# Optimization experiments

Measured on AMD Instinct MI355X. Metric: run time of the kernel, lower is better.

## Reference

```python
import jax, jax.numpy as jnp
import numpy as np

B = 8
RESOLUTIONS = [65, 129, 257, 513, 1025]
NUM_POINTS = [0, 4096, 16384, 65536, 262144]
CLIP_MIN = -1e9
FINAL = 1025          # last resolution (both axes)
B_MIN, B_MAX = -1.0, 1.0
BALANCE = 0.5


def setup_inputs() -> dict:
    key = jax.random.key(0)
    k1, k2, k3, k4 = jax.random.split(key, 4)
    return {
        "w1": jax.random.normal(k1, (2, 256), jnp.float32),
        "b1": jax.random.normal(k2, (256,), jnp.float32),
        "w2": jax.random.normal(k3, (256, 1), jnp.float32),
        "b2": jax.random.normal(k4, (1,), jnp.float32),
    }


def _interp_bilinear_ac(x, H, W):
    """F.interpolate(..., mode='bilinear', align_corners=True). x: [B, C, h, w]."""
    b, c, h, w = x.shape
    ys = jnp.linspace(0.0, h - 1.0, H)
    xs = jnp.linspace(0.0, w - 1.0, W)
    y0 = jnp.floor(ys).astype(jnp.int32)
    y1 = jnp.minimum(y0 + 1, h - 1)
    wy = ys - y0
    x0 = jnp.floor(xs).astype(jnp.int32)
    x1 = jnp.minimum(x0 + 1, w - 1)
    wx = xs - x0
    # interpolate rows, then columns
    top = x[:, :, y0, :] * (1.0 - wy)[None, None, :, None] + x[:, :, y1, :] * wy[None, None, :, None]
    return top[:, :, :, x0] * (1.0 - wx) + top[:, :, :, x1] * wx


def _batch_eval(coords, w1, b1, w2, b2):
    """coords: [B, N, 2] in final-resolution pixel space (align_corners=False mapping).
    Returns occupancy [B, N] (C == 1)."""
    coords2d = coords / FINAL + 0.5 / FINAL                 # normalize to [0, 1]
    p = coords2d * (B_MAX - B_MIN) + B_MIN                  # [B, N, 2] in world coords
    h = jax.nn.relu(jnp.einsum('bnd,dh->bnh', p, w1) + b1)  # [B, N, 256]
    occ = jax.nn.sigmoid(jnp.einsum('bnh,ho->bno', h, w2) + b2)
    return occ[..., 0]


def reference(w1, b1, w2, b2):
    occ = None
    for i, res in enumerate(RESOLUTIONS):
        if i == 0:
            # init_coords: grid of res x res points spanning [0, FINAL-1]
            xs = jnp.linspace(0.0, FINAL - 1.0, res)
            gy, gx = jnp.meshgrid(xs, xs, indexing='ij')          # y rows, x cols
            coords = jnp.stack([gx.ravel(), gy.ravel()], axis=-1)  # [N, 2] (x, y)
            coords = jnp.broadcast_to(coords, (B, res * res, 2))
            o = _batch_eval(coords, w1, b1, w2, b2)               # [B, N]
            occ = o.reshape(B, 1, res, res)                       # [B, C, H, W]
        else:
            occ = _interp_bilinear_ac(occ, res, res)
            npt = NUM_POINTS[i]
            if npt <= 0:
                continue
            # uncertainty = -|occ - balance_value|
            unc = -jnp.abs(occ - BALANCE)                          # [B, 1, H, W]
            flat_unc = unc.reshape(B, res * res)
            scores, idx = jax.lax.top_k(flat_unc, npt)             # [B, npt]
            px = (idx % res).astype(jnp.float32)
            py = (idx // res).astype(jnp.float32)
            stride = (FINAL - 1.0) / (res - 1.0)
            coords = jnp.stack([px, py], axis=-1) * stride         # [B, npt, 2]
            new_vals = _batch_eval(coords, w1, b1, w2, b2)         # [B, npt]
            occ_flat = occ.reshape(B, res * res)
            old_vals = jnp.take_along_axis(occ_flat, idx, axis=1)
            vals = jnp.where(scores >= CLIP_MIN, new_vals, old_vals)
            occ_flat = jax.vmap(lambda o, i2, v: o.at[i2].set(v))(occ_flat, idx, vals)
            occ = occ_flat.reshape(B, 1, res, res)
    return occ
```

## Files before the change

### kernel.cpp

```cpp
#include <hip/hip_runtime.h>
#include <stdint.h>

#define HID 256
#define NMAXPIX (1025 * 1025)
#define NREP 8
#define NSEG 2048
#define SELMAX 2112

#define HISTA_OFF 0
#define HISTB_OFF 16384
#define HISTC_OFF 32768
#define SCAL_OFF  40960
#define TIC_OFF   41024
#define STAGE_U32 43072

__device__ __forceinline__ float mlp_eval4(float wx, float wy,
                                           const float4* __restrict__ w1x,
                                           const float4* __restrict__ w1y,
                                           const float4* __restrict__ vb1,
                                           const float4* __restrict__ vw2, float b2v) {
    const float C0 = (float)(0.5 / 1025.0);
    float px = (wx / 1025.0f + C0) * 2.0f - 1.0f;
    float py = (wy / 1025.0f + C0) * 2.0f - 1.0f;
    float a0 = 0.f, a1 = 0.f, a2 = 0.f, a3 = 0.f;
#pragma unroll 8
    for (int q = 0; q < HID / 4; ++q) {
        float4 a = w1x[q], b = w1y[q], c = vb1[q], d = vw2[q];
        float h0 = px * a.x + py * b.x + c.x;
        float h1 = px * a.y + py * b.y + c.y;
        float h2 = px * a.z + py * b.z + c.z;
        float h3 = px * a.w + py * b.w + c.w;
        h0 = h0 > 0.f ? h0 : 0.f;
        h1 = h1 > 0.f ? h1 : 0.f;
        h2 = h2 > 0.f ? h2 : 0.f;
        h3 = h3 > 0.f ? h3 : 0.f;
        a0 += h0 * d.x;
        a1 += h1 * d.y;
        a2 += h2 * d.z;
        a3 += h3 * d.w;
    }
    float x = ((a0 + a1) + (a2 + a3)) + b2v;
    float r;
    if (x >= 0.f) { r = 1.0f / (1.0f + expf(-x)); }
    else { float e = expf(x); r = e / (1.0f + e); }
    return r;
}

__device__ __forceinline__ uint32_t block_exscan_256(uint32_t v, volatile uint32_t* lds4) {
    int lane = threadIdx.x & 63, w = threadIdx.x >> 6;
    uint32_t inc = v;
#pragma unroll
    for (int d = 1; d < 64; d <<= 1) {
        uint32_t o = (uint32_t)__shfl_up((int)inc, d, 64);
        if (lane >= d) inc += o;
    }
    if (lane == 63) lds4[w] = inc;
    __syncthreads();
    uint32_t woff = 0;
    for (int i = 0; i < w; ++i) woff += lds4[i];
    return woff + inc - v;
}

__device__ void scan_generic(const uint32_t* __restrict__ hist, int NB, int nrep,
                             uint32_t rem_in, uint32_t prefix_in, int shift,
                             uint32_t* outp, uint32_t* outr,
                             volatile uint32_t* lds4, volatile uint32_t* ldspair) {
    int tid = threadIdx.x;
    int C = NB >> 8;
    int b0 = NB - (tid + 1) * C;
    uint32_t cnts[8];
#pragma unroll
    for (int k = 0; k < 8; ++k) cnts[k] = 0;
    for (int rep = 0; rep < nrep; ++rep) {
        const uint4* p = (const uint4*)(hist + (size_t)rep * NB + b0);
#pragma unroll
        for (int g = 0; g < 2; ++g) {
            if (g * 4 < C) {
                uint4 v = p[g];
                cnts[g * 4 + 0] += v.x;
                cnts[g * 4 + 1] += v.y;
                cnts[g * 4 + 2] += v.z;
                cnts[g * 4 + 3] += v.w;
            }
        }
    }
    uint32_t ssum = 0;
    for (int k = 0; k < C; ++k) ssum += cnts[k];
    uint32_t excl = block_exscan_256(ssum, lds4);
    uint32_t run = excl;
    for (int k = 0; k < C; ++k) {
        uint32_t c = cnts[C - 1 - k];
        if (rem_in > run && rem_in <= run + c) {
            ldspair[0] = (prefix_in << shift) | (uint32_t)(b0 + C - 1 - k);
            ldspair[1] = rem_in - run;
        }
        run += c;
    }
    __syncthreads();
    *outp = ldspair[0];
    *outr = ldspair[1];
}

__device__ __forceinline__ void hist_add(uint32_t* lh, uint32_t bin, bool act, int lane) {
    unsigned long long m = __ballot(act);
    if (m) {
        int leader = __ffsll(m) - 1;
        uint32_t lbin = (uint32_t)__shfl((int)bin, leader, 64);
        unsigned long long smk = __ballot(act && bin == lbin);
        if (smk == m) {
            if (lane == leader) atomicAdd(&lh[lbin], (uint32_t)__popcll(m));
        } else if (act) {
            atomicAdd(&lh[bin], 1u);
        }
    }
}

__device__ __forceinline__ float up2x(const float* __restrict__ in, int rp, int r, int n) {
    int i = n / r, j = n % r;
    int i2 = i >> 1, j2 = j >> 1;
    float v;
    if ((i & 1) == 0) {
        if ((j & 1) == 0) {
            v = in[i2 * rp + j2];
        } else {
            float a = in[i2 * rp + j2], b = in[i2 * rp + j2 + 1];
            v = a * 0.5f + b * 0.5f;
        }
    } else {
        if ((j & 1) == 0) {
            float a = in[i2 * rp + j2], b = in[(i2 + 1) * rp + j2];
            v = a * 0.5f + b * 0.5f;
        } else {
            float a = in[i2 * rp + j2],      c = in[i2 * rp + j2 + 1];
            float b = in[(i2 + 1) * rp + j2], d = in[(i2 + 1) * rp + j2 + 1];
            float t1 = a * 0.5f + b * 0.5f;
            float t2 = c * 0.5f + d * 0.5f;
            v = t1 * 0.5f + t2 * 0.5f;
        }
    }
    return v;
}

__global__ __launch_bounds__(256) void k_eval0z(const float* __restrict__ w1, const float* __restrict__ b1,
                                                const float* __restrict__ w2, const float* __restrict__ b2,
                                                float* __restrict__ occ, uint32_t* __restrict__ zbuf, int zcount) {
    __shared__ alignas(16) float sw1[2 * HID];
    __shared__ alignas(16) float sb1[HID];
    __shared__ alignas(16) float sw2[HID];
    int tid = threadIdx.x;
    for (int i = tid; i < 2 * HID; i += 256) sw1[i] = w1[i];
    sb1[tid] = b1[tid];
    sw2[tid] = w2[tid];
    __syncthreads();
    int gtid = blockIdx.x * 256 + tid;
    int nthreads = gridDim.x * 256;
    for (int i = gtid; i < zcount; i += nthreads) zbuf[i] = 0;
    for (int n = gtid; n < 65 * 65; n += nthreads) {
        int i = n / 65, j = n % 65;
        occ[n] = mlp_eval4(16.0f * (float)j, 16.0f * (float)i,
                           (const float4*)sw1, (const float4*)(sw1 + HID),
                           (const float4*)sb1, (const float4*)sw2, b2[0]);
    }
}

__global__ __launch_bounds__(256) void k_upkey(const float* __restrict__ in, int rp,
                                               float* __restrict__ outg, int r, int nb, int bstride,
                                               uint32_t* __restrict__ keys,
                                               uint32_t* __restrict__ histA) {
    __shared__ uint32_t hist[2048];
    int tid = threadIdx.x;
    for (int k = tid; k < 2048; k += 256) hist[k] = 0;
    __syncthreads();
    int N = r * r;
    int lane = tid & 63;
    int gstride = gridDim.x * 256;
    for (int n0 = blockIdx.x * 256; n0 < N; n0 += gstride) {
        int n = n0 + tid;
        bool act = n < N;
        uint32_t key = 0;
        if (act) {
            float v = up2x(in, rp, r, n);
            for (int k = 0; k < nb; ++k) outg[(size_t)k * bstride + n] = v;
            float unc = -fabsf(v - 0.5f);
            uint32_t u = __float_as_uint(unc);
            key = (u & 0x80000000u) ? ~u : (u | 0x80000000u);
            keys[n] = key;
        }
        hist_add(hist, key >> 21, act, lane);
    }
    __syncthreads();
    uint32_t* myrep = histA + (size_t)(blockIdx.x & (NREP - 1)) * 2048;
    for (int k = tid; k < 2048; k += 256) {
        uint32_t c = hist[k];
        if (c) atomicAdd(&myrep[k], c);
    }
}

__global__ __launch_bounds__(256) void k_histmid(const uint32_t* __restrict__ keys, int N,
                                                 const uint32_t* __restrict__ prevHist,
                                                 uint32_t* __restrict__ scal,
                                                 int useNpt, uint32_t npt, int scalInIdx, int shift,
                                                 int scalOutIdx,
                                                 int fshift, int bshift, uint32_t bmask,
                                                 uint32_t* __restrict__ outHist, int NBout) {
    __shared__ uint32_t lh[2048];
    __shared__ uint32_t lds4[4];
    __shared__ uint32_t ldspair[2];
    int tid = threadIdx.x, lane = tid & 63;
    uint32_t rem_in = useNpt ? npt : scal[scalInIdx + 1];
    uint32_t pfx_in = useNpt ? 0u  : scal[scalInIdx];
    uint32_t pfx, rem;
    scan_generic(prevHist, 2048, NREP, rem_in, pfx_in, shift, &pfx, &rem, lds4, ldspair);
    if (blockIdx.x == 0 && tid == 0) { scal[scalOutIdx] = pfx; scal[scalOutIdx + 1] = rem; }
    for (int k = tid; k < 2048; k += 256) lh[k] = 0;
    __syncthreads();
    int gstride = gridDim.x * 256;
    for (int base = blockIdx.x * 256; base < N; base += gstride) {
        int n = base + tid;
        bool inb = n < N;
        uint32_t key = inb ? keys[n] : 0u;
        bool flt = inb && ((key >> fshift) == pfx);
        uint32_t bin = (key >> bshift) & bmask;
        hist_add(lh, bin, flt, lane);
    }
    __syncthreads();
    uint32_t* myrep = outHist + (size_t)(blockIdx.x & (NREP - 1)) * NBout;
    for (int k = tid; k < NBout; k += 256) {
        uint32_t c = lh[k];
        if (c) atomicAdd(&myrep[k], c);
    }
}

__global__ __launch_bounds__(256, 2) void k_segsel(
        const uint32_t* __restrict__ keys, int N, int seglen,
        const uint32_t* __restrict__ histC,
        const uint32_t* __restrict__ scal,
        uint32_t* __restrict__ tic,
        int r, float stride,
        float* __restrict__ occ, int nb, int bstride,
        const float* __restrict__ w1, const float* __restrict__ b1,
        const float* __restrict__ w2, const float* __restrict__ b2) {
    __shared__ alignas(16) float sw1[2 * HID];
    __shared__ alignas(16) float sb1[HID];
    __shared__ alignas(16) float sw2[HID];
    __shared__ uint32_t selcnt;
    __shared__ uint32_t selidx[SELMAX];
    __shared__ uint32_t lds4[4];
    __shared__ uint32_t ldspair[2];
    __shared__ uint32_t wtc[4];
    __shared__ uint32_t s_excl;
    int tid = threadIdx.x, lane = tid & 63, w = tid >> 6;
    for (int i = tid; i < 2 * HID; i += 256) sw1[i] = w1[i];
    sb1[tid] = b1[tid];
    sw2[tid] = w2[tid];
    if (tid == 0) { selcnt = 0; s_excl = 0; }

    uint32_t rem2 = scal[3], pfx2 = scal[2];
    uint32_t K, t;
    scan_generic(histC, 1024, NREP, rem2, pfx2, 10, &K, &t, lds4, ldspair);

    int wv = blockIdx.x * 4 + w;
    int s0 = wv * seglen;
    int s1 = s0 + seglen; if (s1 > N) s1 = N;
    uint32_t tcnt = 0;
    for (int base = s0; base < s1; base += 64) {
        int n = base + lane;
        if (n < s1) tcnt += (keys[n] == K) ? 1u : 0u;
    }
#pragma unroll
    for (int d = 32; d; d >>= 1) tcnt += (uint32_t)__shfl_down((int)tcnt, d, 64);
    if (lane == 0) wtc[w] = tcnt;
    __syncthreads();
    uint32_t agg = wtc[0] + wtc[1] + wtc[2] + wtc[3];
    uint32_t intra = 0;
    for (int i = 0; i < w; ++i) intra += wtc[i];

    if (tid == 0) {
        uint32_t st = (blockIdx.x == 0) ? ((2u << 30) | agg) : ((1u << 30) | agg);
        __hip_atomic_store(&tic[blockIdx.x], st, __ATOMIC_RELAXED, __HIP_MEMORY_SCOPE_AGENT);
    }
    if (blockIdx.x > 0 && w == 0) {
        uint32_t excl = 0;
        int b = (int)blockIdx.x - 1;
        for (;;) {
            int mine = b - lane;
            bool active = (mine >= 0);
            uint32_t f = 0;
            if (active) {
                f = __hip_atomic_load(&tic[mine], __ATOMIC_RELAXED, __HIP_MEMORY_SCOPE_AGENT);
                int spins = 0;
                while ((f >> 30) == 0u && spins < 1000) {
                    __builtin_amdgcn_s_sleep(2);
                    f = __hip_atomic_load(&tic[mine], __ATOMIC_RELAXED, __HIP_MEMORY_SCOPE_AGENT);
                    ++spins;
                }
                if ((f >> 30) == 0u) {
                    int ms0 = mine * seglen;
                    int ms1 = ms0 + seglen; if (ms1 > N) ms1 = N;
                    uint32_t c = 0;
                    for (int n2 = ms0; n2 < ms1; ++n2) c += (keys[n2] == K) ? 1u : 0u;
                    f = (1u << 30) | c;
                }
            }
            unsigned long long incm = __ballot(active && (f >> 30) == 2u);
            uint32_t val;
            bool done = (incm != 0ull);
            if (done) {
                int l2 = __ffsll(incm) - 1;
                val = (lane <= l2) ? (f & 0x3FFFFFFFu) : 0u;
            } else {
                val = active ? (f & 0x3FFFFFFFu) : 0u;
            }
#pragma unroll
            for (int d = 32; d; d >>= 1) val += (uint32_t)__shfl_down((int)val, d, 64);
            val = (uint32_t)__shfl((int)val, 0, 64);
            excl += val;
            if (done) break;
            if (b < 64) break;
            b -= 64;
        }
        if (lane == 0) {
            __hip_atomic_store(&tic[blockIdx.x], (2u << 30) | (excl + agg),
                               __ATOMIC_RELAXED, __HIP_MEMORY_SCOPE_AGENT);
            s_excl = excl;
        }
    }
    __syncthreads();
    uint32_t tie_run = s_excl + intra;

    unsigned long long lowmask = (lane == 63) ? ~0ull >> 1 : ((1ull << lane) - 1ull);
    for (int base = s0; base < s1; base += 64) {
        int n = base + lane;
        bool inb = n < s1;
        uint32_t key = inb ? keys[n] : 0u;
        bool gt = inb && (key > K);
        bool tie = inb && (key == K);
        unsigned long long tm = __ballot(tie);
        uint32_t trank = tie_run + (uint32_t)__popcll(tm & lowmask);
        bool sel = gt || (tie && trank < t);
        unsigned long long smk = __ballot(sel);
        if (smk) {
            int leader = __ffsll(smk) - 1;
            uint32_t wbase = 0;
            if (lane == leader) wbase = atomicAdd(&selcnt, (uint32_t)__popcll(smk));
            wbase = (uint32_t)__shfl((int)wbase, leader, 64);
            if (sel) selidx[wbase + (uint32_t)__popcll(smk & lowmask)] = (uint32_t)n;
        }
        tie_run += (uint32_t)__popcll(tm);
    }
    __syncthreads();

    uint32_t cnt = selcnt;
    float vb2 = b2[0];
    const float4* w1x = (const float4*)sw1;
    const float4* w1y = (const float4*)(sw1 + HID);
    const float4* vb1 = (const float4*)sb1;
    const float4* vw2 = (const float4*)sw2;
    const float C0 = (float)(0.5 / 1025.0);
    for (uint32_t bb = 0; bb < cnt; bb += 512) {
        uint32_t i0 = bb + tid, i1 = bb + tid + 256;
        bool v0 = i0 < cnt, v1 = i1 < cnt;
        int nA = v0 ? (int)selidx[i0] : 0;
        int nB = v1 ? (int)selidx[i1] : 0;
        int iA = nA / r, jA = nA % r;
        int iB = nB / r, jB = nB % r;
        float pxA = ((stride * (float)jA) / 1025.0f + C0) * 2.0f - 1.0f;
        float pyA = ((stride * (float)iA) / 1025.0f + C0) * 2.0f - 1.0f;
        float pxB = ((stride * (float)jB) / 1025.0f + C0) * 2.0f - 1.0f;
        float pyB = ((stride * (float)iB) / 1025.0f + C0) * 2.0f - 1.0f;
        float4 A0 = {0, 0, 0, 0}, A1 = {0, 0, 0, 0};
#pragma unroll 4
        for (int q = 0; q < HID / 4; ++q) {
            float4 a = w1x[q], b = w1y[q], c = vb1[q], d = vw2[q];
            {
                float h0 = pxA * a.x + pyA * b.x + c.x;
                float h1 = pxA * a.y + pyA * b.y + c.y;
                float h2 = pxA * a.z + pyA * b.z + c.z;
                float h3 = pxA * a.w + pyA * b.w + c.w;
                h0 = h0 > 0.f ? h0 : 0.f;
                h1 = h1 > 0.f ? h1 : 0.f;
                h2 = h2 > 0.f ? h2 : 0.f;
                h3 = h3 > 0.f ? h3 : 0.f;
                A0.x += h0 * d.x; A0.y += h1 * d.y;
                A0.z += h2 * d.z; A0.w += h3 * d.w;
            }
            {
                float h0 = pxB * a.x + pyB * b.x + c.x;
                float h1 = pxB * a.y + pyB * b.y + c.y;
                float h2 = pxB * a.z + pyB * b.z + c.z;
                float h3 = pxB * a.w + pyB * b.w + c.w;
                h0 = h0 > 0.f ? h0 : 0.f;
                h1 = h1 > 0.f ? h1 : 0.f;
                h2 = h2 > 0.f ? h2 : 0.f;
                h3 = h3 > 0.f ? h3 : 0.f;
                A1.x += h0 * d.x; A1.y += h1 * d.y;
                A1.z += h2 * d.z; A1.w += h3 * d.w;
            }
        }
        if (v0) {
            float x = ((A0.x + A0.y) + (A0.z + A0.w)) + vb2;
            float rr;
            if (x >= 0.f) { rr = 1.0f / (1.0f + expf(-x)); }
            else { float e = expf(x); rr = e / (1.0f + e); }
            for (int k = 0; k < nb; ++k) occ[(size_t)k * bstride + nA] = rr;
        }
        if (v1) {
            float x = ((A1.x + A1.y) + (A1.z + A1.w)) + vb2;
            float rr;
            if (x >= 0.f) { rr = 1.0f / (1.0f + expf(-x)); }
            else { float e = expf(x); rr = e / (1.0f + e); }
            for (int k = 0; k < nb; ++k) occ[(size_t)k * bstride + nB] = rr;
        }
    }
}

__global__ __launch_bounds__(256) void k_bcast(const float* __restrict__ src, float* __restrict__ dst, int N) {
    int q = blockIdx.x * 256 + threadIdx.x;
    int n = q * 4;
    if (n + 3 < N) {
        float4 v = *(const float4*)(src + n);
#pragma unroll
        for (int k = 0; k < 8; ++k) *(float4*)(dst + (size_t)k * N + n) = v;
    } else if (n < N) {
        for (int m = n; m < N; ++m) {
            float v = src[m];
#pragma unroll
            for (int k = 0; k < 8; ++k) dst[(size_t)k * N + m] = v;
        }
    }
}

extern "C" void kernel_launch(void* const* d_in, const int* in_sizes, int n_in,
                              void* d_out, int out_size, void* d_ws, size_t ws_size,
                              hipStream_t stream) {
    const float* w1 = (const float*)d_in[0];
    const float* b1 = (const float*)d_in[1];
    const float* w2 = (const float*)d_in[2];
    const float* b2 = (const float*)d_in[3];
    float* out = (float*)d_out;

    const size_t A = (((size_t)NMAXPIX * 4) + 255) & ~(size_t)255;
    const size_t SMALL_BYTES = (size_t)4 * STAGE_U32 * 4;
    const size_t need = 3 * A + SMALL_BYTES;

    int fused8 = (ws_size >= need);
    char* base = fused8 ? (char*)d_ws : (char*)d_out;
    float* buf0 = (float*)(base);
    float* buf1 = (float*)(base + A);
    uint32_t* keys = (uint32_t*)(base + 2 * A);
    uint32_t* smallb = (uint32_t*)(base + 3 * A);

    k_eval0z<<<dim3(512), dim3(256), 0, stream>>>(w1, b1, w2, b2, buf0, smallb, 4 * STAGE_U32);

    const int resA[5] = {65, 129, 257, 513, 1025};
    const int nptA[5] = {0, 4096, 16384, 65536, 262144};
    float* cur = buf0;
    float* nxt = buf1;
    for (int s = 1; s < 5; ++s) {
        int rp = resA[s - 1], r = resA[s];
        int N = r * r;
        uint32_t npt = (uint32_t)nptA[s];
        uint32_t* sm    = smallb + (size_t)(s - 1) * STAGE_U32;
        uint32_t* histA = sm + HISTA_OFF;
        uint32_t* histB = sm + HISTB_OFF;
        uint32_t* histC = sm + HISTC_OFF;
        uint32_t* scal  = sm + SCAL_OFF;
        uint32_t* tic   = sm + TIC_OFF;
        int nb1 = (N + 255) / 256;
        int nbu = nb1 < 1024 ? nb1 : 1024;
        int seglen = (N + NSEG - 1) / NSEG;
        float stride = 1024.0f / (float)(r - 1);

        int last = (s == 4);
        float* stage_out = (last && fused8) ? out : nxt;
        int nb = (last && fused8) ? 8 : 1;
        int bstride = (last && fused8) ? NMAXPIX : 0;

        k_upkey<<<dim3(nbu), dim3(256), 0, stream>>>(cur, rp, stage_out, r, nb, bstride, keys, histA);
        k_histmid<<<dim3(512), dim3(256), 0, stream>>>(keys, N, histA, scal, 1, npt, 0, 0,
                                                       0, 21, 10, 0x7FFu, histB, 2048);
        k_histmid<<<dim3(512), dim3(256), 0, stream>>>(keys, N, histB, scal, 0, 0u, 0, 11,
                                                       2, 10, 0, 0x3FFu, histC, 1024);
        k_segsel<<<dim3(NSEG / 4), dim3(256), 0, stream>>>(keys, N, seglen, histC, scal, tic,
                                                           r, stride, stage_out, nb, bstride,
                                                           w1, b1, w2, b2);
        if (!(last && fused8)) { float* tmp = cur; cur = nxt; nxt = tmp; }
    }
    if (!fused8) {
        k_bcast<<<dim3(((NMAXPIX + 3) / 4 + 255) / 256), dim3(256), 0, stream>>>(cur, out, NMAXPIX);
    }
}
```

Measured before the change: 244.6 us.

## Fuse stage-1 selection into one persistent kernel; split select and MLP eval

Stage 1 (129x129) now runs as a single 64-block kernel. It performs upsampling, the three radix-histogram passes, tie counting and MLP evaluation, using grid-wide atomic counters with spin-wait barriers and a redundant local fallback if the wait times out. This replaces four kernel launches for a small stage. For later stages, the segmented select kernel now only compacts selected indices into a global buffer, and a separate kernel evaluates the MLP over them across the whole grid. The split aims to balance the MLP work across blocks, at the cost of an extra launch and extra global traffic. The spin barriers assume all 64 blocks are co-resident.

```diff
diff --git a/kernel.cpp b/kernel.cpp
--- a/kernel.cpp
+++ b/kernel.cpp
@@ -13,6 +13,22 @@
 #define SCAL_OFF  40960
 #define TIC_OFF   41024
 #define STAGE_U32 43072
+
+#define R1P 65
+#define R1  129
+#define N1  (129 * 129)
+#define NPT1 4096u
+#define NSEG1 256
+#define SEG1 66
+#define B1 64
+#define NREP1 4
+
+__device__ __forceinline__ uint32_t aload(const uint32_t* p) {
+    return __hip_atomic_load(p, __ATOMIC_RELAXED, __HIP_MEMORY_SCOPE_AGENT);
+}
+__device__ __forceinline__ void astore(uint32_t* p, uint32_t v) {
+    __hip_atomic_store(p, v, __ATOMIC_RELAXED, __HIP_MEMORY_SCOPE_AGENT);
+}
 
 __device__ __forceinline__ float mlp_eval4(float wx, float wy,
                                            const float4* __restrict__ w1x,
@@ -101,6 +117,36 @@
     *outr = ldspair[1];
 }
 
+__device__ void scan_atomic(const uint32_t* __restrict__ hist, int NB, int nrep,
+                            uint32_t rem_in, uint32_t prefix_in, int shift,
+                            uint32_t* outp, uint32_t* outr,
+                            volatile uint32_t* lds4, volatile uint32_t* ldspair) {
+    int tid = threadIdx.x;
+    int C = NB >> 8;
+    int b0 = NB - (tid + 1) * C;
+    uint32_t cnts[8];
+#pragma unroll
+    for (int k = 0; k < 8; ++k) cnts[k] = 0;
+    for (int rep = 0; rep < nrep; ++rep)
+        for (int k = 0; k < C; ++k)
+            cnts[k] += aload(&hist[(size_t)rep * NB + b0 + k]);
+    uint32_t ssum = 0;
+    for (int k = 0; k < C; ++k) ssum += cnts[k];
+    uint32_t excl = block_exscan_256(ssum, lds4);
+    uint32_t run = excl;
+    for (int k = 0; k < C; ++k) {
+        uint32_t c = cnts[C - 1 - k];
+        if (rem_in > run && rem_in <= run + c) {
+            ldspair[0] = (prefix_in << shift) | (uint32_t)(b0 + C - 1 - k);
+            ldspair[1] = rem_in - run;
+        }
+        run += c;
+    }
+    __syncthreads();
+    *outp = ldspair[0];
+    *outr = ldspair[1];
+}
+
 __device__ __forceinline__ void hist_add(uint32_t* lh, uint32_t bin, bool act, int lane) {
     unsigned long long m = __ballot(act);
     if (m) {
@@ -141,6 +187,31 @@
     return v;
 }
 
+__device__ __forceinline__ uint32_t mkkey(float v) {
+    float unc = -fabsf(v - 0.5f);
+    uint32_t u = __float_as_uint(unc);
+    return (u & 0x80000000u) ? ~u : (u | 0x80000000u);
+}
+
+__device__ __forceinline__ uint32_t key_of(const float* __restrict__ in, int rp, int r, int n) {
+    return mkkey(up2x(in, rp, r, n));
+}
+
+__device__ bool wait_ctr(uint32_t* ctr, uint32_t target, volatile uint32_t* sflag) {
+    if (threadIdx.x == 0) {
+        uint32_t d = aload(ctr);
+        int sp = 0;
+        while (d < target && sp < 20000) {
+            __builtin_amdgcn_s_sleep(4);
+            d = aload(ctr);
+            ++sp;
+        }
+        *sflag = (d >= target) ? 1u : 0u;
+    }
+    __syncthreads();
+    return *sflag != 0;
+}
+
 __global__ __launch_bounds__(256) void k_eval0z(const float* __restrict__ w1, const float* __restrict__ b1,
                                                 const float* __restrict__ w2, const float* __restrict__ b2,
                                                 float* __restrict__ occ, uint32_t* __restrict__ zbuf, int zcount) {
@@ -163,6 +234,201 @@
     }
 }
 
+__global__ __launch_bounds__(256) void k_s1all(const float* __restrict__ in,
+                                               float* __restrict__ outg,
+                                               uint32_t* __restrict__ keys,
+                                               uint32_t* __restrict__ sm,
+                                               const float* __restrict__ w1, const float* __restrict__ b1,
+                                               const float* __restrict__ w2, const float* __restrict__ b2) {
+    __shared__ alignas(16) float sw1[2 * HID];
+    __shared__ alignas(16) float sb1[HID];
+    __shared__ alignas(16) float sw2[HID];
+    __shared__ alignas(16) uint32_t lh[2048];
+    __shared__ uint32_t selidx[SELMAX];
+    __shared__ uint32_t selcnt;
+    __shared__ uint32_t lds4[4];
+    __shared__ uint32_t ldspair[2];
+    __shared__ uint32_t sflag;
+
+    uint32_t* histA = sm + HISTA_OFF;
+    uint32_t* histB = sm + HISTB_OFF;
+    uint32_t* histC = sm + HISTC_OFF;
+    uint32_t* scal  = sm + SCAL_OFF;
+    uint32_t* tic   = sm + TIC_OFF;
+
+    const int tid = threadIdx.x, lane = tid & 63, w = tid >> 6;
+    for (int i = tid; i < 2 * HID; i += 256) sw1[i] = w1[i];
+    sb1[tid] = b1[tid];
+    sw2[tid] = w2[tid];
+    if (tid == 0) selcnt = 0;
+    for (int k = tid; k < 2048; k += 256) lh[k] = 0;
+    __syncthreads();
+
+    for (int n0 = blockIdx.x * 256; n0 < N1; n0 += B1 * 256) {
+        int n = n0 + tid;
+        bool act = n < N1;
+        uint32_t key = 0;
+        if (act) {
+            float v = up2x(in, R1P, R1, n);
+            outg[n] = v;
+            key = mkkey(v);
+            astore(&keys[n], key);
+        }
+        hist_add(lh, key >> 21, act, lane);
+    }
+    __syncthreads();
+    {
+        uint32_t* rep = histA + (size_t)(blockIdx.x & (NREP1 - 1)) * 2048;
+        for (int k = tid; k < 2048; k += 256) { uint32_t c = lh[k]; if (c) atomicAdd(&rep[k], c); }
+    }
+    __syncthreads();
+    if (tid == 0) __hip_atomic_fetch_add(&scal[8], 1u, __ATOMIC_RELAXED, __HIP_MEMORY_SCOPE_AGENT);
+
+    uint32_t pfx1, rem1;
+    if (wait_ctr(&scal[8], B1, &sflag)) {
+        scan_atomic(histA, 2048, NREP1, NPT1, 0u, 0, &pfx1, &rem1, lds4, ldspair);
+    } else {
+        for (int k = tid; k < 2048; k += 256) lh[k] = 0;
+        __syncthreads();
+        for (int n0 = 0; n0 < N1; n0 += 256) {
+            int n = n0 + tid; bool act = n < N1;
+            uint32_t key = act ? key_of(in, R1P, R1, n) : 0u;
+            hist_add(lh, key >> 21, act, lane);
+        }
+        __syncthreads();
+        scan_generic(lh, 2048, 1, NPT1, 0u, 0, &pfx1, &rem1, lds4, ldspair);
+    }
+
+    for (int k = tid; k < 2048; k += 256) lh[k] = 0;
+    __syncthreads();
+    for (int n0 = blockIdx.x * 256; n0 < N1; n0 += B1 * 256) {
+        int n = n0 + tid;
+        bool act = n < N1;
+        uint32_t key = act ? aload(&keys[n]) : 0u;
+        bool flt = act && ((key >> 21) == pfx1);
+        hist_add(lh, (key >> 10) & 0x7FFu, flt, lane);
+    }
+    __syncthreads();
+    {
+        uint32_t* rep = histB + (size_t)(blockIdx.x & (NREP1 - 1)) * 2048;
+        for (int k = tid; k < 2048; k += 256) { uint32_t c = lh[k]; if (c) atomicAdd(&rep[k], c); }
+    }
+    __syncthreads();
+    if (tid == 0) __hip_atomic_fetch_add(&scal[9], 1u, __ATOMIC_RELAXED, __HIP_MEMORY_SCOPE_AGENT);
+
+    uint32_t pfx2, rem2;
+    if (wait_ctr(&scal[9], B1, &sflag)) {
+        scan_atomic(histB, 2048, NREP1, rem1, pfx1, 11, &pfx2, &rem2, lds4, ldspair);
+    } else {
+        for (int k = tid; k < 2048; k += 256) lh[k] = 0;
+        __syncthreads();
+        for (int n0 = 0; n0 < N1; n0 += 256) {
+            int n = n0 + tid; bool act = n < N1;
+            uint32_t key = act ? key_of(in, R1P, R1, n) : 0u;
+            bool flt = act && ((key >> 21) == pfx1);
+            hist_add(lh, (key >> 10) & 0x7FFu, flt, lane);
+        }
+        __syncthreads();
+        scan_generic(lh, 2048, 1, rem1, pfx1, 11, &pfx2, &rem2, lds4, ldspair);
+    }
+
+    for (int k = tid; k < 2048; k += 256) lh[k] = 0;
+    __syncthreads();
+    for (int n0 = blockIdx.x * 256; n0 < N1; n0 += B1 * 256) {
+        int n = n0 + tid;
+        bool act = n < N1;
+        uint32_t key = act ? aload(&keys[n]) : 0u;
+        bool flt = act && ((key >> 10) == pfx2);
+        hist_add(lh, key & 0x3FFu, flt, lane);
+    }
+    __syncthreads();
+    {
+        uint32_t* rep = histC + (size_t)(blockIdx.x & (NREP1 - 1)) * 1024;
+        for (int k = tid; k < 1024; k += 256) { uint32_t c = lh[k]; if (c) atomicAdd(&rep[k], c); }
+    }
+    __syncthreads();
+    if (tid == 0) __hip_atomic_fetch_add(&scal[10], 1u, __ATOMIC_RELAXED, __HIP_MEMORY_SCOPE_AGENT);
+
+    uint32_t K, t;
+    if (wait_ctr(&scal[10], B1, &sflag)) {
+        scan_atomic(histC, 1024, NREP1, rem2, pfx2, 10, &K, &t, lds4, ldspair);
+    } else {
+        for (int k = tid; k < 2048; k += 256) lh[k] = 0;
+        __syncthreads();
+        for (int n0 = 0; n0 < N1; n0 += 256) {
+            int n = n0 + tid; bool act = n < N1;
+            uint32_t key = act ? key_of(in, R1P, R1, n) : 0u;
+            bool flt = act && ((key >> 10) == pfx2);
+            hist_add(lh, key & 0x3FFu, flt, lane);
+        }
+        __syncthreads();
+        scan_generic(lh, 1024, 1, rem2, pfx2, 10, &K, &t, lds4, ldspair);
+    }
+
+    int wv = blockIdx.x * 4 + w;
+    int s0 = wv * SEG1;
+    int s1e = s0 + SEG1; if (s1e > N1) s1e = N1;
+    uint32_t tcnt = 0;
+    for (int base = s0; base < s1e; base += 64) {
+        int n = base + lane;
+        if (n < s1e) tcnt += (aload(&keys[n]) == K) ? 1u : 0u;
+    }
+#pragma unroll
+    for (int d = 32; d; d >>= 1) tcnt += (uint32_t)__shfl_down((int)tcnt, d, 64);
+    if (lane == 0) astore(&tic[wv], tcnt);
+    __syncthreads();
+    if (tid == 0) __hip_atomic_fetch_add(&scal[11], 1u, __ATOMIC_RELAXED, __HIP_MEMORY_SCOPE_AGENT);
+
+    uint32_t tp = 0;
+    if (wait_ctr(&scal[11], B1, &sflag)) {
+        for (int i = lane; i < wv; i += 64) tp += aload(&tic[i]);
+    } else {
+        for (int i = lane; i < wv; i += 64) {
+            int a0 = i * SEG1, a1 = a0 + SEG1; if (a1 > N1) a1 = N1;
+            uint32_t c = 0;
+            for (int n2 = a0; n2 < a1; ++n2) c += (key_of(in, R1P, R1, n2) == K) ? 1u : 0u;
+            tp += c;
+        }
+    }
+#pragma unroll
+    for (int d = 32; d; d >>= 1) tp += (uint32_t)__shfl_down((int)tp, d, 64);
+    tp = (uint32_t)__shfl((int)tp, 0, 64);
+
+    uint32_t tie_run = tp;
+    unsigned long long lowmask = (lane == 63) ? ~0ull >> 1 : ((1ull << lane) - 1ull);
+    for (int base = s0; base < s1e; base += 64) {
+        int n = base + lane;
+        bool inb = n < s1e;
+        uint32_t key = inb ? aload(&keys[n]) : 0u;
+        bool gt = inb && (key > K);
+        bool tie = inb && (key == K);
+        unsigned long long tm = __ballot(tie);
+        uint32_t trank = tie_run + (uint32_t)__popcll(tm & lowmask);
+        bool sel = gt || (tie && trank < t);
+        unsigned long long smk = __ballot(sel);
+        if (smk) {
+            int leader = __ffsll(smk) - 1;
+            uint32_t wbase = 0;
+            if (lane == leader) wbase = atomicAdd(&selcnt, (uint32_t)__popcll(smk));
+            wbase = (uint32_t)__shfl((int)wbase, leader, 64);
+            if (sel) selidx[wbase + (uint32_t)__popcll(smk & lowmask)] = (uint32_t)n;
+        }
+        tie_run += (uint32_t)__popcll(tm);
+    }
+    __syncthreads();
+
+    uint32_t cnt = selcnt;
+    float vb2 = b2[0];
+    for (uint32_t i = tid; i < cnt; i += 256) {
+        int n = (int)selidx[i];
+        int ii = n / R1, jj = n % R1;
+        float rr = mlp_eval4(8.0f * (float)jj, 8.0f * (float)ii,
+                             (const float4*)sw1, (const float4*)(sw1 + HID),
+                             (const float4*)sb1, (const float4*)sw2, vb2);
+        outg[n] = rr;
+    }
+}
+
 __global__ __launch_bounds__(256) void k_upkey(const float* __restrict__ in, int rp,
                                                float* __restrict__ outg, int r, int nb, int bstride,
                                                uint32_t* __restrict__ keys,
@@ -181,9 +447,7 @@
         if (act) {
             float v = up2x(in, rp, r, n);
             for (int k = 0; k < nb; ++k) outg[(size_t)k * bstride + n] = v;
-            float unc = -fabsf(v - 0.5f);
-            uint32_t u = __float_as_uint(unc);
-            key = (u & 0x80000000u) ? ~u : (u | 0x80000000u);
+            key = mkkey(v);
             keys[n] = key;
         }
         hist_add(hist, key >> 21, act, lane);
@@ -231,28 +495,21 @@
     }
 }
 
-__global__ __launch_bounds__(256, 2) void k_segsel(
+__global__ __launch_bounds__(256, 2) void k_segselc(
         const uint32_t* __restrict__ keys, int N, int seglen,
         const uint32_t* __restrict__ histC,
         const uint32_t* __restrict__ scal,
         uint32_t* __restrict__ tic,
-        int r, float stride,
-        float* __restrict__ occ, int nb, int bstride,
-        const float* __restrict__ w1, const float* __restrict__ b1,
-        const float* __restrict__ w2, const float* __restrict__ b2) {
-    __shared__ alignas(16) float sw1[2 * HID];
-    __shared__ alignas(16) float sb1[HID];
-    __shared__ alignas(16) float sw2[HID];
+        uint32_t* __restrict__ gcnt,
+        uint32_t* __restrict__ selbuf) {
     __shared__ uint32_t selcnt;
     __shared__ uint32_t selidx[SELMAX];
     __shared__ uint32_t lds4[4];
     __shared__ uint32_t ldspair[2];
     __shared__ uint32_t wtc[4];
     __shared__ uint32_t s_excl;
+    __shared__ uint32_t gbase;
     int tid = threadIdx.x, lane = tid & 63, w = tid >> 6;
-    for (int i = tid; i < 2 * HID; i += 256) sw1[i] = w1[i];
-    sb1[tid] = b1[tid];
-    sw2[tid] = w2[tid];
     if (tid == 0) { selcnt = 0; s_excl = 0; }
 
     uint32_t rem2 = scal[3], pfx2 = scal[2];
@@ -277,7 +534,7 @@
 
     if (tid == 0) {
         uint32_t st = (blockIdx.x == 0) ? ((2u << 30) | agg) : ((1u << 30) | agg);
-        __hip_atomic_store(&tic[blockIdx.x], st, __ATOMIC_RELAXED, __HIP_MEMORY_SCOPE_AGENT);
+        astore(&tic[blockIdx.x], st);
     }
     if (blockIdx.x > 0 && w == 0) {
         uint32_t excl = 0;
@@ -287,11 +544,11 @@
             bool active = (mine >= 0);
             uint32_t f = 0;
             if (active) {
-                f = __hip_atomic_load(&tic[mine], __ATOMIC_RELAXED, __HIP_MEMORY_SCOPE_AGENT);
+                f = aload(&tic[mine]);
                 int spins = 0;
                 while ((f >> 30) == 0u && spins < 1000) {
                     __builtin_amdgcn_s_sleep(2);
-                    f = __hip_atomic_load(&tic[mine], __ATOMIC_RELAXED, __HIP_MEMORY_SCOPE_AGENT);
+                    f = aload(&tic[mine]);
                     ++spins;
                 }
                 if ((f >> 30) == 0u) {
@@ -320,8 +577,7 @@
             b -= 64;
         }
         if (lane == 0) {
-            __hip_atomic_store(&tic[blockIdx.x], (2u << 30) | (excl + agg),
-                               __ATOMIC_RELAXED, __HIP_MEMORY_SCOPE_AGENT);
+            astore(&tic[blockIdx.x], (2u << 30) | (excl + agg));
             s_excl = excl;
         }
     }
@@ -350,67 +606,34 @@
     }
     __syncthreads();
 
-    uint32_t cnt = selcnt;
+    if (tid == 0) gbase = atomicAdd(gcnt, selcnt);
+    __syncthreads();
+    uint32_t cnt = selcnt, gb = gbase;
+    for (uint32_t i = tid; i < cnt; i += 256) selbuf[gb + i] = selidx[i];
+}
+
+__global__ __launch_bounds__(256) void k_evalsel(const uint32_t* __restrict__ selbuf, int npt,
+                                                 int r, float stride,
+                                                 float* __restrict__ occ, int nb, int bstride,
+                                                 const float* __restrict__ w1, const float* __restrict__ b1,
+                                                 const float* __restrict__ w2, const float* __restrict__ b2) {
+    __shared__ alignas(16) float sw1[2 * HID];
+    __shared__ alignas(16) float sb1[HID];
+    __shared__ alignas(16) float sw2[HID];
+    int tid = threadIdx.x;
+    for (int i = tid; i < 2 * HID; i += 256) sw1[i] = w1[i];
+    sb1[tid] = b1[tid];
+    sw2[tid] = w2[tid];
+    __syncthreads();
     float vb2 = b2[0];
-    const float4* w1x = (const float4*)sw1;
-    const float4* w1y = (const float4*)(sw1 + HID);
-    const float4* vb1 = (const float4*)sb1;
-    const float4* vw2 = (const float4*)sw2;
-    const float C0 = (float)(0.5 / 1025.0);
-    for (uint32_t bb = 0; bb < cnt; bb += 512) {
-        uint32_t i0 = bb + tid, i1 = bb + tid + 256;
-        bool v0 = i0 < cnt, v1 = i1 < cnt;
-        int nA = v0 ? (int)selidx[i0] : 0;
-        int nB = v1 ? (int)selidx[i1] : 0;
-        int iA = nA / r, jA = nA % r;
-        int iB = nB / r, jB = nB % r;
-        float pxA = ((stride * (float)jA) / 1025.0f + C0) * 2.0f - 1.0f;
-        float pyA = ((stride * (float)iA) / 1025.0f + C0) * 2.0f - 1.0f;
-        float pxB = ((stride * (float)jB) / 1025.0f + C0) * 2.0f - 1.0f;
-        float pyB = ((stride * (float)iB) / 1025.0f + C0) * 2.0f - 1.0f;
-        float4 A0 = {0, 0, 0, 0}, A1 = {0, 0, 0, 0};
-#pragma unroll 4
-        for (int q = 0; q < HID / 4; ++q) {
-            float4 a = w1x[q], b = w1y[q], c = vb1[q], d = vw2[q];
-            {
-                float h0 = pxA * a.x + pyA * b.x + c.x;
-                float h1 = pxA * a.y + pyA * b.y + c.y;
-                float h2 = pxA * a.z + pyA * b.z + c.z;
-                float h3 = pxA * a.w + pyA * b.w + c.w;
-                h0 = h0 > 0.f ? h0 : 0.f;
-                h1 = h1 > 0.f ? h1 : 0.f;
-                h2 = h2 > 0.f ? h2 : 0.f;
-                h3 = h3 > 0.f ? h3 : 0.f;
-                A0.x += h0 * d.x; A0.y += h1 * d.y;
-                A0.z += h2 * d.z; A0.w += h3 * d.w;
-            }
-            {
-                float h0 = pxB * a.x + pyB * b.x + c.x;
-                float h1 = pxB * a.y + pyB * b.y + c.y;
-                float h2 = pxB * a.z + pyB * b.z + c.z;
-                float h3 = pxB * a.w + pyB * b.w + c.w;
-                h0 = h0 > 0.f ? h0 : 0.f;
-                h1 = h1 > 0.f ? h1 : 0.f;
-                h2 = h2 > 0.f ? h2 : 0.f;
-                h3 = h3 > 0.f ? h3 : 0.f;
-                A1.x += h0 * d.x; A1.y += h1 * d.y;
-                A1.z += h2 * d.z; A1.w += h3 * d.w;
-            }
-        }
-        if (v0) {
-            float x = ((A0.x + A0.y) + (A0.z + A0.w)) + vb2;
-            float rr;
-            if (x >= 0.f) { rr = 1.0f / (1.0f + expf(-x)); }
-            else { float e = expf(x); rr = e / (1.0f + e); }
-            for (int k = 0; k < nb; ++k) occ[(size_t)k * bstride + nA] = rr;
-        }
-        if (v1) {
-            float x = ((A1.x + A1.y) + (A1.z + A1.w)) + vb2;
-            float rr;
-            if (x >= 0.f) { rr = 1.0f / (1.0f + expf(-x)); }
-            else { float e = expf(x); rr = e / (1.0f + e); }
-            for (int k = 0; k < nb; ++k) occ[(size_t)k * bstride + nB] = rr;
-        }
+    int gs = gridDim.x * 256;
+    for (int i = blockIdx.x * 256 + tid; i < npt; i += gs) {
+        int n = (int)selbuf[i];
+        int ii = n / r, jj = n % r;
+        float rr = mlp_eval4(stride * (float)jj, stride * (float)ii,
+                             (const float4*)sw1, (const float4*)(sw1 + HID),
+                             (const float4*)sb1, (const float4*)sw2, vb2);
+        for (int k = 0; k < nb; ++k) occ[(size_t)k * bstride + n] = rr;
     }
 }
 
@@ -441,7 +664,8 @@
 
     const size_t A = (((size_t)NMAXPIX * 4) + 255) & ~(size_t)255;
     const size_t SMALL_BYTES = (size_t)4 * STAGE_U32 * 4;
-    const size_t need = 3 * A + SMALL_BYTES;
+    const size_t SELB_BYTES = ((size_t)262144 * 4 + 255) & ~(size_t)255;
+    const size_t need = 3 * A + SMALL_BYTES + SELB_BYTES;
 
     int fused8 = (ws_size >= need);
     char* base = fused8 ? (char*)d_ws : (char*)d_out;
@@ -449,14 +673,17 @@
     float* buf1 = (float*)(base + A);
     uint32_t* keys = (uint32_t*)(base + 2 * A);
     uint32_t* smallb = (uint32_t*)(base + 3 * A);
+    uint32_t* selbuf = (uint32_t*)(base + 3 * A + SMALL_BYTES);
 
     k_eval0z<<<dim3(512), dim3(256), 0, stream>>>(w1, b1, w2, b2, buf0, smallb, 4 * STAGE_U32);
+
+    k_s1all<<<dim3(B1), dim3(256), 0, stream>>>(buf0, buf1, keys, smallb, w1, b1, w2, b2);
 
     const int resA[5] = {65, 129, 257, 513, 1025};
     const int nptA[5] = {0, 4096, 16384, 65536, 262144};
-    float* cur = buf0;
-    float* nxt = buf1;
-    for (int s = 1; s < 5; ++s) {
+    float* cur = buf1;
+    float* nxt = buf0;
+    for (int s = 2; s < 5; ++s) {
         int rp = resA[s - 1], r = resA[s];
         int N = r * r;
         uint32_t npt = (uint32_t)nptA[s];
@@ -476,14 +703,17 @@
         int nb = (last && fused8) ? 8 : 1;
         int bstride = (last && fused8) ? NMAXPIX : 0;
 
+        int nbe = (int)((npt + 255) / 256); if (nbe > 512) nbe = 512;
+
         k_upkey<<<dim3(nbu), dim3(256), 0, stream>>>(cur, rp, stage_out, r, nb, bstride, keys, histA);
         k_histmid<<<dim3(512), dim3(256), 0, stream>>>(keys, N, histA, scal, 1, npt, 0, 0,
                                                        0, 21, 10, 0x7FFu, histB, 2048);
         k_histmid<<<dim3(512), dim3(256), 0, stream>>>(keys, N, histB, scal, 0, 0u, 0, 11,
                                                        2, 10, 0, 0x3FFu, histC, 1024);
-        k_segsel<<<dim3(NSEG / 4), dim3(256), 0, stream>>>(keys, N, seglen, histC, scal, tic,
-                                                           r, stride, stage_out, nb, bstride,
-                                                           w1, b1, w2, b2);
+        k_segselc<<<dim3(NSEG / 4), dim3(256), 0, stream>>>(keys, N, seglen, histC, scal, tic,
+                                                            scal + 6, selbuf);
+        k_evalsel<<<dim3(nbe), dim3(256), 0, stream>>>(selbuf, (int)npt, r, stride,
+                                                       stage_out, nb, bstride, w1, b1, w2, b2);
         if (!(last && fused8)) { float* tmp = cur; cur = nxt; nxt = tmp; }
     }
     if (!fused8) {
```

Result: no change. 240.6 us (-1.6%).

## Split selection and MLP evaluation into separate kernels with compacted index buffer

Applied to the files above, without the earlier changes.

The fused select-and-evaluate kernel is split in two. The first kernel computes an exact global output position for each selected pixel by carrying both tie and greater-than counts in a 64-bit decoupled-lookback prefix, then writes indices into a dense global buffer. A second kernel evaluates the MLP over that buffer with a load-balanced grid. Before, each block evaluated only the points that landed in its own segments, so MLP work was spread unevenly. The change adds an extra launch and a global round trip for the indices, and doubles the size of the lookback payload.

```diff
diff --git a/kernel.cpp b/kernel.cpp
--- a/kernel.cpp
+++ b/kernel.cpp
@@ -5,7 +5,6 @@
 #define NMAXPIX (1025 * 1025)
 #define NREP 8
 #define NSEG 2048
-#define SELMAX 2112
 
 #define HISTA_OFF 0
 #define HISTB_OFF 16384
@@ -13,6 +12,13 @@
 #define SCAL_OFF  40960
 #define TIC_OFF   41024
 #define STAGE_U32 43072
+
+__device__ __forceinline__ unsigned long long aload64(const unsigned long long* p) {
+    return __hip_atomic_load(p, __ATOMIC_RELAXED, __HIP_MEMORY_SCOPE_AGENT);
+}
+__device__ __forceinline__ void astore64(unsigned long long* p, unsigned long long v) {
+    __hip_atomic_store(p, v, __ATOMIC_RELAXED, __HIP_MEMORY_SCOPE_AGENT);
+}
 
 __device__ __forceinline__ float mlp_eval4(float wx, float wy,
                                            const float4* __restrict__ w1x,
@@ -141,6 +147,12 @@
     return v;
 }
 
+__device__ __forceinline__ uint32_t mkkey(float v) {
+    float unc = -fabsf(v - 0.5f);
+    uint32_t u = __float_as_uint(unc);
+    return (u & 0x80000000u) ? ~u : (u | 0x80000000u);
+}
+
 __global__ __launch_bounds__(256) void k_eval0z(const float* __restrict__ w1, const float* __restrict__ b1,
                                                 const float* __restrict__ w2, const float* __restrict__ b2,
                                                 float* __restrict__ occ, uint32_t* __restrict__ zbuf, int zcount) {
@@ -181,9 +193,7 @@
         if (act) {
             float v = up2x(in, rp, r, n);
             for (int k = 0; k < nb; ++k) outg[(size_t)k * bstride + n] = v;
-            float unc = -fabsf(v - 0.5f);
-            uint32_t u = __float_as_uint(unc);
-            key = (u & 0x80000000u) ? ~u : (u | 0x80000000u);
+            key = mkkey(v);
             keys[n] = key;
         }
         hist_add(hist, key >> 21, act, lane);
@@ -231,29 +241,18 @@
     }
 }
 
-__global__ __launch_bounds__(256, 2) void k_segsel(
+__global__ __launch_bounds__(256, 2) void k_segselc(
         const uint32_t* __restrict__ keys, int N, int seglen,
         const uint32_t* __restrict__ histC,
         const uint32_t* __restrict__ scal,
-        uint32_t* __restrict__ tic,
-        int r, float stride,
-        float* __restrict__ occ, int nb, int bstride,
-        const float* __restrict__ w1, const float* __restrict__ b1,
-        const float* __restrict__ w2, const float* __restrict__ b2) {
-    __shared__ alignas(16) float sw1[2 * HID];
-    __shared__ alignas(16) float sb1[HID];
-    __shared__ alignas(16) float sw2[HID];
-    __shared__ uint32_t selcnt;
-    __shared__ uint32_t selidx[SELMAX];
+        unsigned long long* __restrict__ tic64,
+        uint32_t* __restrict__ selbuf) {
     __shared__ uint32_t lds4[4];
     __shared__ uint32_t ldspair[2];
-    __shared__ uint32_t wtc[4];
-    __shared__ uint32_t s_excl;
+    __shared__ uint32_t wtc[4], wgc[4];
+    __shared__ uint32_t s_excl_t, s_excl_g;
     int tid = threadIdx.x, lane = tid & 63, w = tid >> 6;
-    for (int i = tid; i < 2 * HID; i += 256) sw1[i] = w1[i];
-    sb1[tid] = b1[tid];
-    sw2[tid] = w2[tid];
-    if (tid == 0) { selcnt = 0; s_excl = 0; }
+    if (tid == 0) { s_excl_t = 0; s_excl_g = 0; }
 
     uint32_t rem2 = scal[3], pfx2 = scal[2];
     uint32_t K, t;
@@ -262,71 +261,94 @@
     int wv = blockIdx.x * 4 + w;
     int s0 = wv * seglen;
     int s1 = s0 + seglen; if (s1 > N) s1 = N;
-    uint32_t tcnt = 0;
+    uint32_t tcnt = 0, gcnt2 = 0;
     for (int base = s0; base < s1; base += 64) {
         int n = base + lane;
-        if (n < s1) tcnt += (keys[n] == K) ? 1u : 0u;
-    }
-#pragma unroll
-    for (int d = 32; d; d >>= 1) tcnt += (uint32_t)__shfl_down((int)tcnt, d, 64);
-    if (lane == 0) wtc[w] = tcnt;
-    __syncthreads();
-    uint32_t agg = wtc[0] + wtc[1] + wtc[2] + wtc[3];
-    uint32_t intra = 0;
-    for (int i = 0; i < w; ++i) intra += wtc[i];
+        if (n < s1) {
+            uint32_t key = keys[n];
+            tcnt += (key == K) ? 1u : 0u;
+            gcnt2 += (key > K) ? 1u : 0u;
+        }
+    }
+#pragma unroll
+    for (int d = 32; d; d >>= 1) {
+        tcnt += (uint32_t)__shfl_down((int)tcnt, d, 64);
+        gcnt2 += (uint32_t)__shfl_down((int)gcnt2, d, 64);
+    }
+    if (lane == 0) { wtc[w] = tcnt; wgc[w] = gcnt2; }
+    __syncthreads();
+    uint32_t agg_t = wtc[0] + wtc[1] + wtc[2] + wtc[3];
+    uint32_t agg_g = wgc[0] + wgc[1] + wgc[2] + wgc[3];
+    uint32_t intra_t = 0, intra_g = 0;
+    for (int i = 0; i < w; ++i) { intra_t += wtc[i]; intra_g += wgc[i]; }
 
     if (tid == 0) {
-        uint32_t st = (blockIdx.x == 0) ? ((2u << 30) | agg) : ((1u << 30) | agg);
-        __hip_atomic_store(&tic[blockIdx.x], st, __ATOMIC_RELAXED, __HIP_MEMORY_SCOPE_AGENT);
+        unsigned long long pay = ((unsigned long long)agg_t << 24) | (unsigned long long)agg_g;
+        unsigned long long st = (blockIdx.x == 0) ? ((2ull << 62) | pay) : ((1ull << 62) | pay);
+        astore64(&tic64[blockIdx.x], st);
     }
     if (blockIdx.x > 0 && w == 0) {
-        uint32_t excl = 0;
+        uint32_t excl_t = 0, excl_g = 0;
         int b = (int)blockIdx.x - 1;
         for (;;) {
             int mine = b - lane;
             bool active = (mine >= 0);
-            uint32_t f = 0;
+            unsigned long long f = 0;
             if (active) {
-                f = __hip_atomic_load(&tic[mine], __ATOMIC_RELAXED, __HIP_MEMORY_SCOPE_AGENT);
+                f = aload64(&tic64[mine]);
                 int spins = 0;
-                while ((f >> 30) == 0u && spins < 1000) {
+                while ((f >> 62) == 0ull && spins < 1000) {
                     __builtin_amdgcn_s_sleep(2);
-                    f = __hip_atomic_load(&tic[mine], __ATOMIC_RELAXED, __HIP_MEMORY_SCOPE_AGENT);
+                    f = aload64(&tic64[mine]);
                     ++spins;
                 }
-                if ((f >> 30) == 0u) {
-                    int ms0 = mine * seglen;
-                    int ms1 = ms0 + seglen; if (ms1 > N) ms1 = N;
-                    uint32_t c = 0;
-                    for (int n2 = ms0; n2 < ms1; ++n2) c += (keys[n2] == K) ? 1u : 0u;
-                    f = (1u << 30) | c;
+                if ((f >> 62) == 0ull) {
+                    int ms0 = mine * 4 * seglen;
+                    int ms1 = ms0 + 4 * seglen; if (ms1 > N) ms1 = N;
+                    uint32_t ct = 0, cg = 0;
+                    for (int n2 = ms0; n2 < ms1; ++n2) {
+                        uint32_t key = keys[n2];
+                        ct += (key == K) ? 1u : 0u;
+                        cg += (key > K) ? 1u : 0u;
+                    }
+                    f = (1ull << 62) | ((unsigned long long)ct << 24) | (unsigned long long)cg;
                 }
             }
-            unsigned long long incm = __ballot(active && (f >> 30) == 2u);
-            uint32_t val;
+            unsigned long long incm = __ballot(active && (f >> 62) == 2ull);
+            uint32_t vt, vg;
             bool done = (incm != 0ull);
             if (done) {
                 int l2 = __ffsll(incm) - 1;
-                val = (lane <= l2) ? (f & 0x3FFFFFFFu) : 0u;
+                vt = (lane <= l2) ? (uint32_t)((f >> 24) & 0xFFFFFFull) : 0u;
+                vg = (lane <= l2) ? (uint32_t)(f & 0xFFFFFFull) : 0u;
             } else {
-                val = active ? (f & 0x3FFFFFFFu) : 0u;
+                vt = active ? (uint32_t)((f >> 24) & 0xFFFFFFull) : 0u;
+                vg = active ? (uint32_t)(f & 0xFFFFFFull) : 0u;
             }
 #pragma unroll
-            for (int d = 32; d; d >>= 1) val += (uint32_t)__shfl_down((int)val, d, 64);
-            val = (uint32_t)__shfl((int)val, 0, 64);
-            excl += val;
+            for (int d = 32; d; d >>= 1) {
+                vt += (uint32_t)__shfl_down((int)vt, d, 64);
+                vg += (uint32_t)__shfl_down((int)vg, d, 64);
+            }
+            vt = (uint32_t)__shfl((int)vt, 0, 64);
+            vg = (uint32_t)__shfl((int)vg, 0, 64);
+            excl_t += vt;
+            excl_g += vg;
             if (done) break;
             if (b < 64) break;
             b -= 64;
         }
         if (lane == 0) {
-            __hip_atomic_store(&tic[blockIdx.x], (2u << 30) | (excl + agg),
-                               __ATOMIC_RELAXED, __HIP_MEMORY_SCOPE_AGENT);
-            s_excl = excl;
-        }
-    }
-    __syncthreads();
-    uint32_t tie_run = s_excl + intra;
+            unsigned long long pay = ((unsigned long long)(excl_t + agg_t) << 24)
+                                   | (unsigned long long)(excl_g + agg_g);
+            astore64(&tic64[blockIdx.x], (2ull << 62) | pay);
+            s_excl_t = excl_t;
+            s_excl_g = excl_g;
+        }
+    }
+    __syncthreads();
+    uint32_t tie_run = s_excl_t + intra_t;
+    uint32_t gt_run  = s_excl_g + intra_g;
 
     unsigned long long lowmask = (lane == 63) ? ~0ull >> 1 : ((1ull << lane) - 1ull);
     for (int base = s0; base < s1; base += 64) {
@@ -336,32 +358,45 @@
         bool gt = inb && (key > K);
         bool tie = inb && (key == K);
         unsigned long long tm = __ballot(tie);
-        uint32_t trank = tie_run + (uint32_t)__popcll(tm & lowmask);
-        bool sel = gt || (tie && trank < t);
-        unsigned long long smk = __ballot(sel);
-        if (smk) {
-            int leader = __ffsll(smk) - 1;
-            uint32_t wbase = 0;
-            if (lane == leader) wbase = atomicAdd(&selcnt, (uint32_t)__popcll(smk));
-            wbase = (uint32_t)__shfl((int)wbase, leader, 64);
-            if (sel) selidx[wbase + (uint32_t)__popcll(smk & lowmask)] = (uint32_t)n;
+        unsigned long long gm = __ballot(gt);
+        uint32_t tie_before = tie_run + (uint32_t)__popcll(tm & lowmask);
+        uint32_t gt_before  = gt_run + (uint32_t)__popcll(gm & lowmask);
+        if (gt) {
+            uint32_t tb = tie_before < t ? tie_before : t;
+            selbuf[gt_before + tb] = (uint32_t)n;
+        } else if (tie && tie_before < t) {
+            selbuf[gt_before + tie_before] = (uint32_t)n;
         }
         tie_run += (uint32_t)__popcll(tm);
-    }
-    __syncthreads();
-
-    uint32_t cnt = selcnt;
+        gt_run  += (uint32_t)__popcll(gm);
+    }
+}
+
+__global__ __launch_bounds__(256) void k_evalsel(const uint32_t* __restrict__ selbuf, int npt,
+                                                 int r, float stride,
+                                                 float* __restrict__ occ, int nb, int bstride,
+                                                 const float* __restrict__ w1, const float* __restrict__ b1,
+                                                 const float* __restrict__ w2, const float* __restrict__ b2) {
+    __shared__ alignas(16) float sw1[2 * HID];
+    __shared__ alignas(16) float sb1[HID];
+    __shared__ alignas(16) float sw2[HID];
+    int tid = threadIdx.x;
+    for (int i = tid; i < 2 * HID; i += 256) sw1[i] = w1[i];
+    sb1[tid] = b1[tid];
+    sw2[tid] = w2[tid];
+    __syncthreads();
     float vb2 = b2[0];
     const float4* w1x = (const float4*)sw1;
     const float4* w1y = (const float4*)(sw1 + HID);
     const float4* vb1 = (const float4*)sb1;
     const float4* vw2 = (const float4*)sw2;
     const float C0 = (float)(0.5 / 1025.0);
-    for (uint32_t bb = 0; bb < cnt; bb += 512) {
-        uint32_t i0 = bb + tid, i1 = bb + tid + 256;
-        bool v0 = i0 < cnt, v1 = i1 < cnt;
-        int nA = v0 ? (int)selidx[i0] : 0;
-        int nB = v1 ? (int)selidx[i1] : 0;
+    int gs2 = gridDim.x * 512;
+    for (int bb = blockIdx.x * 512; bb < npt; bb += gs2) {
+        int i0 = bb + tid, i1 = bb + tid + 256;
+        bool v0 = i0 < npt, v1 = i1 < npt;
+        int nA = v0 ? (int)selbuf[i0] : 0;
+        int nB = v1 ? (int)selbuf[i1] : 0;
         int iA = nA / r, jA = nA % r;
         int iB = nB / r, jB = nB % r;
         float pxA = ((stride * (float)jA) / 1025.0f + C0) * 2.0f - 1.0f;
@@ -441,7 +476,8 @@
 
     const size_t A = (((size_t)NMAXPIX * 4) + 255) & ~(size_t)255;
     const size_t SMALL_BYTES = (size_t)4 * STAGE_U32 * 4;
-    const size_t need = 3 * A + SMALL_BYTES;
+    const size_t SELB_BYTES = ((size_t)262144 * 4 + 255) & ~(size_t)255;
+    const size_t need = 3 * A + SMALL_BYTES + SELB_BYTES;
 
     int fused8 = (ws_size >= need);
     char* base = fused8 ? (char*)d_ws : (char*)d_out;
@@ -449,6 +485,7 @@
     float* buf1 = (float*)(base + A);
     uint32_t* keys = (uint32_t*)(base + 2 * A);
     uint32_t* smallb = (uint32_t*)(base + 3 * A);
+    uint32_t* selbuf = (uint32_t*)(base + 3 * A + SMALL_BYTES);
 
     k_eval0z<<<dim3(512), dim3(256), 0, stream>>>(w1, b1, w2, b2, buf0, smallb, 4 * STAGE_U32);
 
@@ -475,15 +512,17 @@
         float* stage_out = (last && fused8) ? out : nxt;
         int nb = (last && fused8) ? 8 : 1;
         int bstride = (last && fused8) ? NMAXPIX : 0;
+        int nbe = (int)((npt + 511) / 512); if (nbe > 512) nbe = 512;
 
         k_upkey<<<dim3(nbu), dim3(256), 0, stream>>>(cur, rp, stage_out, r, nb, bstride, keys, histA);
         k_histmid<<<dim3(512), dim3(256), 0, stream>>>(keys, N, histA, scal, 1, npt, 0, 0,
                                                        0, 21, 10, 0x7FFu, histB, 2048);
         k_histmid<<<dim3(512), dim3(256), 0, stream>>>(keys, N, histB, scal, 0, 0u, 0, 11,
                                                        2, 10, 0, 0x3FFu, histC, 1024);
-        k_segsel<<<dim3(NSEG / 4), dim3(256), 0, stream>>>(keys, N, seglen, histC, scal, tic,
-                                                           r, stride, stage_out, nb, bstride,
-                                                           w1, b1, w2, b2);
+        k_segselc<<<dim3(NSEG / 4), dim3(256), 0, stream>>>(keys, N, seglen, histC, scal,
+                                                            (unsigned long long*)tic, selbuf);
+        k_evalsel<<<dim3(nbe), dim3(256), 0, stream>>>(selbuf, (int)npt, r, stride,
+                                                       stage_out, nb, bstride, w1, b1, w2, b2);
         if (!(last && fused8)) { float* tmp = cur; cur = nxt; nxt = tmp; }
     }
     if (!fused8) {
```

Measured after the change: 229.8 us. 1.06x faster.
